# Kernel tuning notes

Hardware: AMD Instinct MI355X
Metric: run time of the kernel (lower is better)

The kernel has to match this reference:

```python
import math
import jax, jax.numpy as jnp
import numpy as np
from jax import lax

B, H, W = 8, 96, 96
FC, R, P, KS, TOPK = 768, 12, 16, 13, 24
SUP_TH, SUP_MIX, OPEN_K, DIL, NMS = 0.28, 0.8, 3, 3, 3

# prototype anchor metadata (buffers, deterministic)
ORI = jnp.asarray(np.linspace(0.0, math.pi, P + 1)[:-1], jnp.float32)
_lenL = np.array([0.4, 0.7, 1.0, 1.25], np.float32)
_widL = np.array([0.12, 0.18, 0.24, 0.3], np.float32)
LEN = jnp.asarray(_lenL[np.arange(P) % 4])
WID = jnp.asarray(_widL[(np.arange(P) // 4) % 4])
_ax = np.linspace(-1.0, 1.0, KS).astype(np.float32)
_gy, _gx = np.meshgrid(_ax, _ax, indexing='ij')
GX, GY = jnp.asarray(_gx), jnp.asarray(_gy)


def conv2d(x, w, b, pad=0):
    y = lax.conv_general_dilated(x, w, (1, 1), [(pad, pad), (pad, pad)],
                                 dimension_numbers=('NCHW', 'OIHW', 'NCHW'))
    return y + b[None, :, None, None]


def maxpool(x, k):
    p = k // 2
    return lax.reduce_window(x, -jnp.inf, lax.max, (1, 1, k, k), (1, 1, 1, 1),
                             [(0, 0), (0, 0), (p, p), (p, p)])


def avgpool3(x):
    s = lax.reduce_window(x, 0.0, lax.add, (1, 1, 3, 3), (1, 1, 1, 1),
                          [(0, 0), (0, 0), (1, 1), (1, 1)])
    return s / 9.0  # torch count_include_pad=True


def normalize_map(t):
    mn = t.min(axis=(-2, -1), keepdims=True)
    mx = t.max(axis=(-2, -1), keepdims=True)
    return (t - mn) / jnp.maximum(mx - mn, 1e-6)


def binary_open(m, k):
    er = 1.0 - maxpool(1.0 - m, k)
    return jnp.clip(maxpool(er, k), 0.0, 1.0)


def support_mask_fn(carrier_hp, density):
    cs = normalize_map(avgpool3(jnp.abs(carrier_hp)))
    ds = normalize_map(density)
    ev = SUP_MIX * cs + (1.0 - SUP_MIX) * ds
    m = (ev >= SUP_TH).astype(carrier_hp.dtype)
    m = binary_open(m, OPEN_K)
    m = maxpool(m, DIL)
    return jnp.clip(m, 0.0, 1.0)


def setup_inputs() -> dict:
    key = jax.random.key(0)
    ks = jax.random.split(key, 16)
    d = {
        'features': jax.random.normal(ks[0], (B, FC, H, W), jnp.float32),
        'carrier_hp': jax.random.normal(ks[1], (B, 1, H, W), jnp.float32),
        'density': jax.random.uniform(ks[2], (B, 1, H, W), jnp.float32),
        # feature_project: 1x1 conv FC->R, 3x3 conv R->R
        'w1': jax.random.normal(ks[3], (R, FC, 1, 1), jnp.float32) * (1.0 / math.sqrt(FC)),
        'b1': jnp.zeros((R,), jnp.float32),
        'w2': jax.random.normal(ks[4], (R, R, 3, 3), jnp.float32) * (1.0 / math.sqrt(R * 9)),
        'b2': jnp.zeros((R,), jnp.float32),
        # post_mix: 1x1 conv (R+4)->R, 1x1 conv R->FC
        'w3': jax.random.normal(ks[5], (R, R + 4, 1, 1), jnp.float32) * (1.0 / math.sqrt(R + 4)),
        'b3': jnp.zeros((R,), jnp.float32),
        'w4': jax.random.normal(ks[6], (FC, R, 1, 1), jnp.float32) * (1.0 / math.sqrt(R)),
        'b4': jnp.zeros((FC,), jnp.float32),
        'proto': jax.random.normal(ks[7], (P, R), jnp.float32) * 0.02,
    }
    return d


def reference(features, carrier_hp, density, w1, b1, w2, b2, w3, b3, w4, b4, proto):
    gelu = lambda x: jax.nn.gelu(x, approximate=False)
    # 1) feature projection
    proj = gelu(conv2d(gelu(conv2d(features, w1, b1, 0)), w2, b2, 1))  # [B,R,H,W]
    # 2) occupancy + support
    occ = normalize_map(jnp.abs(proj).mean(axis=1, keepdims=True))      # [B,1,H,W]
    sup = support_mask_fn(carrier_hp, density)                          # [B,1,H,W]
    # 3) NMS + top-k anchors
    scores = occ * sup
    local_max = maxpool(scores, NMS)
    peak = ((scores >= local_max) & (scores > 0.05)).astype(scores.dtype)
    flat = (scores * peak).reshape(B, -1)
    vals, idx = lax.top_k(flat, TOPK)                                   # [B,K]
    anchor_map = jnp.zeros_like(flat).at[jnp.arange(B)[:, None], idx].set(vals)
    anchor_map = anchor_map.reshape(B, 1, H, W)
    ys, xs = idx // W, idx % W
    # 4) per-anchor prototype selection
    proj_flat = proj.reshape(B, R, H * W)
    feat_at = jnp.take_along_axis(proj_flat, jnp.broadcast_to(idx[:, None, :], (B, R, TOPK)), axis=2)  # [B,R,K]
    logits = jnp.einsum('brk,pr->bkp', feat_at, proto)
    pidx = jnp.argmax(logits, axis=-1)                                  # [B,K]
    ori, ln, wd = ORI[pidx], LEN[pidx], WID[pidx]
    # 5) oriented Gaussian footprints [B,K,KS,KS]
    c = jnp.cos(ori)[..., None, None]
    s = jnp.sin(ori)[..., None, None]
    xr = c * GX + s * GY
    yr = -s * GX + c * GY
    foot = jnp.exp(-(xr / ln[..., None, None]) ** 2 - (yr / wd[..., None, None]) ** 2)
    foot = foot * vals[..., None, None]
    emb = proto[pidx]                                                   # [B,K,R]
    contrib = emb[:, :, :, None, None] * foot[:, :, None]               # [B,K,R,KS,KS]
    # 6) scatter-stamp onto canvas
    off = jnp.arange(KS) - KS // 2
    yy = ys[:, :, None, None] + off[None, None, :, None]                # [B,K,KS,KS]
    xx = xs[:, :, None, None] + off[None, None, None, :]
    valid = ((yy >= 0) & (yy < H) & (xx >= 0) & (xx < W)).astype(contrib.dtype)
    yyc = jnp.clip(yy, 0, H - 1)
    xxc = jnp.clip(xx, 0, W - 1)

    def stamp(ctr, y2, x2, v):
        c0 = jnp.zeros((R, H, W), ctr.dtype)
        return c0.at[:, y2, x2].add(jnp.transpose(ctr, (1, 0, 2, 3)) * v[None])

    canvas = jax.vmap(stamp)(contrib, yyc, xxc, valid)                  # [B,R,H,W]
    # 7) support-lock + post mix
    canvas = canvas * sup
    extras = jnp.concatenate([occ, sup, anchor_map, normalize_map(density)], axis=1)
    mixed = conv2d(gelu(conv2d(jnp.concatenate([canvas, extras], axis=1), w3, b3, 0)), w4, b4, 0)
    return mixed
```

## Files before the change

### kernel.cpp

```cpp
#include <hip/hip_runtime.h>
#include <math.h>

#define Bn 8
#define Hh 96
#define Ww 96
#define NPIX 9216
#define FCn 768
#define Rr 12
#define Pp 16
#define KSn 13
#define TOPKn 24

__device__ __forceinline__ float gelu_f(float x) {
  return 0.5f * x * (1.0f + erff(x * 0.70710678118654752440f));
}

__global__ __launch_bounds__(256) void k_conv1_part(
    const float* __restrict__ feat, const float* __restrict__ w1,
    float* __restrict__ partial) {
  __shared__ float w1s[192 * 12];
  int s = blockIdx.x & 3;
  int pixblk = blockIdx.x >> 2;
  int c0 = s * 192;
  for (int i = threadIdx.x; i < 192 * 12; i += 256) {
    int c = i / 12, r = i % 12;
    w1s[i] = w1[r * FCn + c0 + c];
  }
  __syncthreads();
  int pix = pixblk * 256 + threadIdx.x;
  int b = pix / NPIX, hw = pix % NPIX;
  const float* fb = feat + (size_t)b * FCn * NPIX + (size_t)c0 * NPIX + hw;
  float acc[12];
#pragma unroll
  for (int r = 0; r < 12; r++) acc[r] = 0.f;
  for (int c = 0; c < 192; c += 8) {
    float f[8];
#pragma unroll
    for (int u = 0; u < 8; u++) f[u] = fb[(size_t)(c + u) * NPIX];
#pragma unroll
    for (int u = 0; u < 8; u++) {
#pragma unroll
      for (int r = 0; r < 12; r++)
        acc[r] = fmaf(f[u], w1s[(c + u) * 12 + r], acc[r]);
    }
  }
  float* outp = partial + (size_t)s * (Bn * Rr * NPIX) +
                (size_t)b * Rr * NPIX + hw;
#pragma unroll
  for (int r = 0; r < 12; r++) outp[(size_t)r * NPIX] = acc[r];
}

__global__ __launch_bounds__(256) void k_bias_gelu(
    const float* __restrict__ partial, const float* __restrict__ b1,
    float* __restrict__ t1) {
  int e = blockIdx.x * 256 + threadIdx.x;
  if (e >= Bn * Rr * NPIX) return;
  int r = (e / NPIX) % Rr;
  const size_t N = (size_t)Bn * Rr * NPIX;
  float v = ((partial[e] + partial[e + N]) + partial[e + 2 * N]) +
            partial[e + 3 * N] + b1[r];
  t1[e] = gelu_f(v);
}

__global__ __launch_bounds__(256) void k_conv2(
    const float* __restrict__ t1, const float* __restrict__ w2,
    const float* __restrict__ b2, const float* __restrict__ carrier,
    float* __restrict__ proj, float* __restrict__ occ_raw,
    float* __restrict__ cs_raw) {
  __shared__ float w2s[Rr * Rr * 9];
  __shared__ float b2s[Rr];
  for (int i = threadIdx.x; i < Rr * Rr * 9; i += 256) w2s[i] = w2[i];
  if (threadIdx.x < Rr) b2s[threadIdx.x] = b2[threadIdx.x];
  __syncthreads();
  int pix = blockIdx.x * 256 + threadIdx.x;
  int b = pix / NPIX, hw = pix % NPIX;
  int y = hw / Ww, x = hw % Ww;
  float acc[12];
#pragma unroll
  for (int r = 0; r < 12; r++) acc[r] = 0.f;
  const float* tb = t1 + (size_t)b * Rr * NPIX;
  for (int ri = 0; ri < Rr; ri++) {
    const float* tc = tb + (size_t)ri * NPIX;
#pragma unroll
    for (int ky = 0; ky < 3; ky++) {
      int yy = y + ky - 1;
      if (yy < 0 || yy >= Hh) continue;
#pragma unroll
      for (int kx = 0; kx < 3; kx++) {
        int xx = x + kx - 1;
        if (xx < 0 || xx >= Ww) continue;
        float v = tc[yy * Ww + xx];
#pragma unroll
        for (int ro = 0; ro < 12; ro++)
          acc[ro] = fmaf(v, w2s[((ro * Rr + ri) * 3 + ky) * 3 + kx], acc[ro]);
      }
    }
  }
  float asum = 0.f;
  float* pb = proj + (size_t)b * Rr * NPIX + hw;
#pragma unroll
  for (int ro = 0; ro < 12; ro++) {
    float g = gelu_f(acc[ro] + b2s[ro]);
    pb[(size_t)ro * NPIX] = g;
    asum += fabsf(g);
  }
  occ_raw[pix] = asum / 12.0f;

  const float* cb = carrier + (size_t)b * NPIX;
  float s9 = 0.f;
  for (int dy = -1; dy <= 1; dy++) {
    int yy = y + dy;
    if (yy < 0 || yy >= Hh) continue;
    for (int dx = -1; dx <= 1; dx++) {
      int xx = x + dx;
      if (xx < 0 || xx >= Ww) continue;
      s9 += fabsf(cb[yy * Ww + xx]);
    }
  }
  cs_raw[pix] = s9 / 9.0f;
}

__global__ __launch_bounds__(256) void k_minmax(
    const float* __restrict__ occ_raw, const float* __restrict__ cs_raw,
    const float* __restrict__ density, float* __restrict__ stats) {
  int a = blockIdx.x / Bn, b = blockIdx.x % Bn;
  const float* src = (a == 0) ? occ_raw : (a == 1) ? cs_raw : density;
  src += (size_t)b * NPIX;
  __shared__ float smn[256], smx[256];
  float mn = INFINITY, mx = -INFINITY;
  for (int p = threadIdx.x; p < NPIX; p += 256) {
    float v = src[p];
    mn = fminf(mn, v);
    mx = fmaxf(mx, v);
  }
  smn[threadIdx.x] = mn;
  smx[threadIdx.x] = mx;
  __syncthreads();
  for (int s = 128; s > 0; s >>= 1) {
    if (threadIdx.x < s) {
      smn[threadIdx.x] = fminf(smn[threadIdx.x], smn[threadIdx.x + s]);
      smx[threadIdx.x] = fmaxf(smx[threadIdx.x], smx[threadIdx.x + s]);
    }
    __syncthreads();
  }
  if (threadIdx.x == 0) {
    stats[(a * Bn + b) * 2 + 0] = smn[0];
    stats[(a * Bn + b) * 2 + 1] = smx[0];
  }
}

__global__ __launch_bounds__(1024) void k_support(
    const float* __restrict__ occ_raw, const float* __restrict__ cs_raw,
    const float* __restrict__ density, const float* __restrict__ stats,
    float* __restrict__ occ, float* __restrict__ ds, float* __restrict__ sup,
    float* __restrict__ scores) {
  __shared__ unsigned char mA[NPIX], mB[NPIX];
  int b = blockIdx.x;
  float omn = stats[(0 * Bn + b) * 2], omx = stats[(0 * Bn + b) * 2 + 1];
  float cmn = stats[(1 * Bn + b) * 2], cmx = stats[(1 * Bn + b) * 2 + 1];
  float dmn = stats[(2 * Bn + b) * 2], dmx = stats[(2 * Bn + b) * 2 + 1];
  float oiv = fmaxf(omx - omn, 1e-6f);
  float civ = fmaxf(cmx - cmn, 1e-6f);
  float div_ = fmaxf(dmx - dmn, 1e-6f);
  float occ9[9];
#pragma unroll
  for (int i = 0; i < 9; i++) {
    int p = threadIdx.x + i * 1024;
    float oc = (occ_raw[b * NPIX + p] - omn) / oiv;
    float cv = (cs_raw[b * NPIX + p] - cmn) / civ;
    float dv = (density[b * NPIX + p] - dmn) / div_;
    occ[b * NPIX + p] = oc;
    ds[b * NPIX + p] = dv;
    occ9[i] = oc;
    float ev = 0.8f * cv + 0.2f * dv;
    mA[p] = (ev >= 0.28f) ? 1 : 0;
  }
  __syncthreads();
#pragma unroll
  for (int i = 0; i < 9; i++) {
    int p = threadIdx.x + i * 1024;
    int y = p / Ww, x = p % Ww;
    unsigned char m = 1;
    for (int dy = -1; dy <= 1; dy++) {
      int yy = y + dy;
      if (yy < 0 || yy >= Hh) continue;
      for (int dx = -1; dx <= 1; dx++) {
        int xx = x + dx;
        if (xx < 0 || xx >= Ww) continue;
        m = (unsigned char)(m & mA[yy * Ww + xx]);
      }
    }
    mB[p] = m;
  }
  __syncthreads();
#pragma unroll
  for (int i = 0; i < 9; i++) {
    int p = threadIdx.x + i * 1024;
    int y = p / Ww, x = p % Ww;
    unsigned char m = 0;
    for (int dy = -1; dy <= 1; dy++) {
      int yy = y + dy;
      if (yy < 0 || yy >= Hh) continue;
      for (int dx = -1; dx <= 1; dx++) {
        int xx = x + dx;
        if (xx < 0 || xx >= Ww) continue;
        m = (unsigned char)(m | mB[yy * Ww + xx]);
      }
    }
    mA[p] = m;
  }
  __syncthreads();
#pragma unroll
  for (int i = 0; i < 9; i++) {
    int p = threadIdx.x + i * 1024;
    int y = p / Ww, x = p % Ww;
    unsigned char m = 0;
    for (int dy = -1; dy <= 1; dy++) {
      int yy = y + dy;
      if (yy < 0 || yy >= Hh) continue;
      for (int dx = -1; dx <= 1; dx++) {
        int xx = x + dx;
        if (xx < 0 || xx >= Ww) continue;
        m = (unsigned char)(m | mA[yy * Ww + xx]);
      }
    }
    float sv = (float)m;
    sup[b * NPIX + p] = sv;
    scores[b * NPIX + p] = occ9[i] * sv;
  }
}

__global__ __launch_bounds__(256) void k_topk(
    const float* __restrict__ scores, float* __restrict__ vals,
    int* __restrict__ idxs, float* __restrict__ anchor) {
  __shared__ float flat[NPIX];
  __shared__ float rv[256];
  __shared__ int ri[256];
  int b = blockIdx.x;
  const float* sc = scores + (size_t)b * NPIX;
  for (int p = threadIdx.x; p < NPIX; p += 256) {
    int y = p / Ww, x = p % Ww;
    float s = sc[p];
    float lm = -INFINITY;
    for (int dy = -1; dy <= 1; dy++) {
      int yy = y + dy;
      if (yy < 0 || yy >= Hh) continue;
      for (int dx = -1; dx <= 1; dx++) {
        int xx = x + dx;
        if (xx < 0 || xx >= Ww) continue;
        lm = fmaxf(lm, sc[yy * Ww + xx]);
      }
    }
    flat[p] = (s >= lm && s > 0.05f) ? s : 0.0f;
  }
  __syncthreads();
  for (int k = 0; k < TOPKn; k++) {
    float bv = -INFINITY;
    int bi = 0x7fffffff;
    for (int p = threadIdx.x; p < NPIX; p += 256) {
      float v = flat[p];
      if (v > bv || (v == bv && p < bi)) {
        bv = v;
        bi = p;
      }
    }
    rv[threadIdx.x] = bv;
    ri[threadIdx.x] = bi;
    __syncthreads();
    for (int s = 128; s > 0; s >>= 1) {
      if (threadIdx.x < s) {
        float ov = rv[threadIdx.x + s];
        int oi = ri[threadIdx.x + s];
        if (ov > rv[threadIdx.x] || (ov == rv[threadIdx.x] && oi < ri[threadIdx.x])) {
          rv[threadIdx.x] = ov;
          ri[threadIdx.x] = oi;
        }
      }
      __syncthreads();
    }
    if (threadIdx.x == 0) {
      vals[b * TOPKn + k] = rv[0];
      idxs[b * TOPKn + k] = ri[0];
      flat[ri[0]] = -2.0f;
      anchor[b * NPIX + ri[0]] = rv[0];
    }
    __syncthreads();
  }
}

__global__ __launch_bounds__(192) void k_stamp(
    const float* __restrict__ proj, const float* __restrict__ proto,
    const float* __restrict__ vals, const int* __restrict__ idxs,
    float* __restrict__ canvas) {
  int b = blockIdx.x / TOPKn, k = blockIdx.x % TOPKn;
  __shared__ float embs[12];
  __shared__ float prm[5];
  __shared__ int ppos[2];
  if (threadIdx.x == 0) {
    int id = idxs[b * TOPKn + k];
    float v = vals[b * TOPKn + k];
    float ft[12];
    for (int r = 0; r < 12; r++)
      ft[r] = proj[(size_t)(b * Rr + r) * NPIX + id];
    float bestL = -INFINITY;
    int bp = 0;
    for (int p = 0; p < Pp; p++) {
      float L = 0.f;
      for (int r = 0; r < 12; r++) L = fmaf(ft[r], proto[p * Rr + r], L);
      if (L > bestL) {
        bestL = L;
        bp = p;
      }
    }
    const float lenL[4] = {0.4f, 0.7f, 1.0f, 1.25f};
    const float widL[4] = {0.12f, 0.18f, 0.24f, 0.3f};
    float ori = (float)((M_PI / 16.0) * (double)bp);
    prm[0] = cosf(ori);
    prm[1] = sinf(ori);
    prm[2] = lenL[bp & 3];
    prm[3] = widL[(bp >> 2) & 3];
    prm[4] = v;
    ppos[0] = id / Ww;
    ppos[1] = id % Ww;
    for (int r = 0; r < 12; r++) embs[r] = proto[bp * Rr + r];
  }
  __syncthreads();
  float v = prm[4];
  if (v <= 0.f) return;
  int t = threadIdx.x;
  if (t >= KSn * KSn) return;
  int i = t / KSn, j = t % KSn;
  float gx = (float)(-1.0 + (double)j * (1.0 / 6.0));
  float gy = (float)(-1.0 + (double)i * (1.0 / 6.0));
  float c = prm[0], s = prm[1];
  float xr = c * gx + s * gy;
  float yr = -s * gx + c * gy;
  float tx = xr / prm[2], ty = yr / prm[3];
  float foot = expf(-(tx * tx) - (ty * ty)) * v;
  int yy = ppos[0] + i - KSn / 2;
  int xx = ppos[1] + j - KSn / 2;
  if (yy < 0 || yy >= Hh || xx < 0 || xx >= Ww) return;
  float* cp = canvas + (size_t)b * Rr * NPIX + yy * Ww + xx;
#pragma unroll
  for (int r = 0; r < 12; r++) atomicAdd(cp + (size_t)r * NPIX, embs[r] * foot);
}

__global__ __launch_bounds__(256) void k_post1(
    const float* __restrict__ canvas, const float* __restrict__ sup,
    const float* __restrict__ occ, const float* __restrict__ anchor,
    const float* __restrict__ ds, const float* __restrict__ w3,
    const float* __restrict__ b3, float* __restrict__ h) {
  __shared__ float w3s[12 * 16], b3s[12];
  for (int i = threadIdx.x; i < 192; i += 256) w3s[i] = w3[i];
  if (threadIdx.x < 12) b3s[threadIdx.x] = b3[threadIdx.x];
  __syncthreads();
  int pix = blockIdx.x * 256 + threadIdx.x;
  int b = pix / NPIX, hw = pix % NPIX;
  float in16[16];
  float sv = sup[pix];
#pragma unroll
  for (int r = 0; r < 12; r++)
    in16[r] = canvas[(size_t)(b * Rr + r) * NPIX + hw] * sv;
  in16[12] = occ[pix];
  in16[13] = sv;
  in16[14] = anchor[pix];
  in16[15] = ds[pix];
  float* hb = h + (size_t)b * Rr * NPIX + hw;
#pragma unroll
  for (int ro = 0; ro < 12; ro++) {
    float acc = 0.f;
#pragma unroll
    for (int ci = 0; ci < 16; ci++)
      acc = fmaf(in16[ci], w3s[ro * 16 + ci], acc);
    hb[(size_t)ro * NPIX] = gelu_f(acc + b3s[ro]);
  }
}

__global__ __launch_bounds__(256) void k_post2(
    const float* __restrict__ h, const float* __restrict__ w4,
    const float* __restrict__ b4, float* __restrict__ out) {
  __shared__ float w4s[16 * 12], b4s[16];
  int bx = blockIdx.x;
  int hwblk = bx % 36;
  int g = (bx / 36) % 48;
  int b = bx / (36 * 48);
  int oc0 = g * 16;
  for (int i = threadIdx.x; i < 192; i += 256) w4s[i] = w4[oc0 * 12 + i];
  if (threadIdx.x < 16) b4s[threadIdx.x] = b4[oc0 + threadIdx.x];
  __syncthreads();
  int hw = hwblk * 256 + threadIdx.x;
  float hreg[12];
  const float* hb = h + (size_t)b * Rr * NPIX + hw;
#pragma unroll
  for (int r = 0; r < 12; r++) hreg[r] = hb[(size_t)r * NPIX];
  float* ob = out + (size_t)(b * FCn + oc0) * NPIX + hw;
#pragma unroll
  for (int j = 0; j < 16; j++) {
    float acc = 0.f;
#pragma unroll
    for (int r = 0; r < 12; r++) acc = fmaf(hreg[r], w4s[j * 12 + r], acc);
    ob[(size_t)j * NPIX] = acc + b4s[j];
  }
}

extern "C" void kernel_launch(void* const* d_in, const int* in_sizes, int n_in,
                              void* d_out, int out_size, void* d_ws,
                              size_t ws_size, hipStream_t stream) {
  const float* features = (const float*)d_in[0];
  const float* carrier = (const float*)d_in[1];
  const float* density = (const float*)d_in[2];
  const float* w1 = (const float*)d_in[3];
  const float* b1 = (const float*)d_in[4];
  const float* w2 = (const float*)d_in[5];
  const float* b2 = (const float*)d_in[6];
  const float* w3 = (const float*)d_in[7];
  const float* b3 = (const float*)d_in[8];
  const float* w4 = (const float*)d_in[9];
  const float* b4 = (const float*)d_in[10];
  const float* proto = (const float*)d_in[11];
  float* out = (float*)d_out;
  float* ws = (float*)d_ws;

  const size_t NT = (size_t)Bn * Rr * NPIX;
  float* t1 = ws;
  float* partial = ws + NT;
  float* proj = partial;
  float* canvas = partial + NT;
  float* h = partial + 2 * NT;
  float* sm = ws + 5 * NT;
  float* occ_raw = sm;
  float* cs_raw = sm + (size_t)Bn * NPIX;
  float* occ = sm + 2 * (size_t)Bn * NPIX;
  float* ds = sm + 3 * (size_t)Bn * NPIX;
  float* sup = sm + 4 * (size_t)Bn * NPIX;
  float* scores = sm + 5 * (size_t)Bn * NPIX;
  float* anchor = sm + 6 * (size_t)Bn * NPIX;
  float* stats = sm + 7 * (size_t)Bn * NPIX;
  float* vals = stats + 64;
  int* idxs = (int*)(vals + Bn * TOPKn);

  k_conv1_part<<<288 * 4, 256, 0, stream>>>(features, w1, partial);
  k_bias_gelu<<<(int)((NT + 255) / 256), 256, 0, stream>>>(partial, b1, t1);
  hipMemsetAsync(canvas, 0, NT * sizeof(float), stream);
  hipMemsetAsync(anchor, 0, (size_t)Bn * NPIX * sizeof(float), stream);
  k_conv2<<<288, 256, 0, stream>>>(t1, w2, b2, carrier, proj, occ_raw, cs_raw);
  k_minmax<<<24, 256, 0, stream>>>(occ_raw, cs_raw, density, stats);
  k_support<<<Bn, 1024, 0, stream>>>(occ_raw, cs_raw, density, stats, occ, ds,
                                     sup, scores);
  k_topk<<<Bn, 256, 0, stream>>>(scores, vals, idxs, anchor);
  k_stamp<<<Bn * TOPKn, 192, 0, stream>>>(proj, proto, vals, idxs, canvas);
  k_post1<<<288, 256, 0, stream>>>(canvas, sup, occ, anchor, ds, w3, b3, h);
  k_post2<<<Bn * 48 * 36, 256, 0, stream>>>(h, w4, b4, out);
}
```

Measured before the change: 651.1 us.

## Compact NMS peak candidates before top-k and use wave-shuffle reductions

The top-k kernel first loads each batch's score map into shared memory and runs the 3x3 local-max suppression from there. Surviving peaks are compacted with a shared atomic counter into a small candidate list (up to 1536 entries). The 24 argmax passes then scan only that list instead of all 9216 pixels. Each pass reduces with 64-lane shuffles and a 4-way cross-wave step instead of an 8-level shared-memory tree with many barriers. If there are too many candidates it falls back to the full scan, and when no positive value remains it writes index 0 rather than the lowest zero pixel, which can change tie behaviour.

Result: faster. 581.7 us (-10.7%).

```diff
diff --git a/kernel.cpp b/kernel.cpp
--- a/kernel.cpp
+++ b/kernel.cpp
@@ -10,6 +10,7 @@
 #define Pp 16
 #define KSn 13
 #define TOPKn 24
+#define CAPc 1536
 
 __device__ __forceinline__ float gelu_f(float x) {
   return 0.5f * x * (1.0f + erff(x * 0.70710678118654752440f));
@@ -234,13 +235,25 @@
     const float* __restrict__ scores, float* __restrict__ vals,
     int* __restrict__ idxs, float* __restrict__ anchor) {
   __shared__ float flat[NPIX];
-  __shared__ float rv[256];
-  __shared__ int ri[256];
+  __shared__ float cval[CAPc];
+  __shared__ int cidx[CAPc];
+  __shared__ int cnt;
+  __shared__ float rv[4];
+  __shared__ int ri[4], rs[4];
   int b = blockIdx.x;
+  const int tid = threadIdx.x;
+  const int lane = tid & 63, wid = tid >> 6;
   const float* sc = scores + (size_t)b * NPIX;
-  for (int p = threadIdx.x; p < NPIX; p += 256) {
+#pragma unroll
+  for (int i = 0; i < NPIX / 256; i++) flat[tid + i * 256] = sc[tid + i * 256];
+  if (tid == 0) cnt = 0;
+  __syncthreads();
+  float pk[NPIX / 256];
+#pragma unroll
+  for (int i = 0; i < NPIX / 256; i++) {
+    int p = tid + i * 256;
     int y = p / Ww, x = p % Ww;
-    float s = sc[p];
+    float s = flat[p];
     float lm = -INFINITY;
     for (int dy = -1; dy <= 1; dy++) {
       int yy = y + dy;
@@ -248,43 +261,122 @@
       for (int dx = -1; dx <= 1; dx++) {
         int xx = x + dx;
         if (xx < 0 || xx >= Ww) continue;
-        lm = fmaxf(lm, sc[yy * Ww + xx]);
-      }
-    }
-    flat[p] = (s >= lm && s > 0.05f) ? s : 0.0f;
-  }
-  __syncthreads();
-  for (int k = 0; k < TOPKn; k++) {
-    float bv = -INFINITY;
-    int bi = 0x7fffffff;
-    for (int p = threadIdx.x; p < NPIX; p += 256) {
-      float v = flat[p];
-      if (v > bv || (v == bv && p < bi)) {
-        bv = v;
-        bi = p;
-      }
-    }
-    rv[threadIdx.x] = bv;
-    ri[threadIdx.x] = bi;
-    __syncthreads();
-    for (int s = 128; s > 0; s >>= 1) {
-      if (threadIdx.x < s) {
-        float ov = rv[threadIdx.x + s];
-        int oi = ri[threadIdx.x + s];
-        if (ov > rv[threadIdx.x] || (ov == rv[threadIdx.x] && oi < ri[threadIdx.x])) {
-          rv[threadIdx.x] = ov;
-          ri[threadIdx.x] = oi;
-        }
+        lm = fmaxf(lm, flat[yy * Ww + xx]);
+      }
+    }
+    pk[i] = (s >= lm && s > 0.05f) ? s : 0.0f;
+  }
+  __syncthreads();
+#pragma unroll
+  for (int i = 0; i < NPIX / 256; i++) {
+    int p = tid + i * 256;
+    flat[p] = pk[i];
+    if (pk[i] > 0.f) {
+      int slot = atomicAdd(&cnt, 1);
+      if (slot < CAPc) {
+        cval[slot] = pk[i];
+        cidx[slot] = p;
+      }
+    }
+  }
+  __syncthreads();
+  const int C = cnt;
+  if (C <= CAPc) {
+    for (int k = 0; k < TOPKn; k++) {
+      float bv = -INFINITY;
+      int bi = 0x7fffffff, bs = -1;
+      for (int j = tid; j < C; j += 256) {
+        float v = cval[j];
+        int pi = cidx[j];
+        if (v > bv || (v == bv && pi < bi)) {
+          bv = v;
+          bi = pi;
+          bs = j;
+        }
+      }
+      for (int off = 32; off > 0; off >>= 1) {
+        float ov = __shfl_xor(bv, off);
+        int oi = __shfl_xor(bi, off);
+        int os = __shfl_xor(bs, off);
+        if (ov > bv || (ov == bv && oi < bi)) {
+          bv = ov;
+          bi = oi;
+          bs = os;
+        }
+      }
+      if (lane == 0) {
+        rv[wid] = bv;
+        ri[wid] = bi;
+        rs[wid] = bs;
       }
       __syncthreads();
-    }
-    if (threadIdx.x == 0) {
-      vals[b * TOPKn + k] = rv[0];
-      idxs[b * TOPKn + k] = ri[0];
-      flat[ri[0]] = -2.0f;
-      anchor[b * NPIX + ri[0]] = rv[0];
-    }
-    __syncthreads();
+      if (tid == 0) {
+        float Bv = rv[0];
+        int Bi = ri[0], Bs = rs[0];
+        for (int w = 1; w < 4; w++) {
+          if (rv[w] > Bv || (rv[w] == Bv && ri[w] < Bi)) {
+            Bv = rv[w];
+            Bi = ri[w];
+            Bs = rs[w];
+          }
+        }
+        if (Bv > 0.f) {
+          vals[b * TOPKn + k] = Bv;
+          idxs[b * TOPKn + k] = Bi;
+          anchor[b * NPIX + Bi] = Bv;
+          cval[Bs] = -INFINITY;
+        } else {
+          vals[b * TOPKn + k] = 0.f;
+          idxs[b * TOPKn + k] = 0;
+        }
+      }
+      __syncthreads();
+    }
+  } else {
+    for (int k = 0; k < TOPKn; k++) {
+      float bv = -INFINITY;
+      int bi = 0x7fffffff;
+      for (int p = tid; p < NPIX; p += 256) {
+        float v = flat[p];
+        if (v > bv || (v == bv && p < bi)) {
+          bv = v;
+          bi = p;
+        }
+      }
+      for (int off = 32; off > 0; off >>= 1) {
+        float ov = __shfl_xor(bv, off);
+        int oi = __shfl_xor(bi, off);
+        if (ov > bv || (ov == bv && oi < bi)) {
+          bv = ov;
+          bi = oi;
+        }
+      }
+      if (lane == 0) {
+        rv[wid] = bv;
+        ri[wid] = bi;
+      }
+      __syncthreads();
+      if (tid == 0) {
+        float Bv = rv[0];
+        int Bi = ri[0];
+        for (int w = 1; w < 4; w++) {
+          if (rv[w] > Bv || (rv[w] == Bv && ri[w] < Bi)) {
+            Bv = rv[w];
+            Bi = ri[w];
+          }
+        }
+        if (Bv > 0.f) {
+          vals[b * TOPKn + k] = Bv;
+          idxs[b * TOPKn + k] = Bi;
+          anchor[b * NPIX + Bi] = Bv;
+          flat[Bi] = -INFINITY;
+        } else {
+          vals[b * TOPKn + k] = 0.f;
+          idxs[b * TOPKn + k] = 0;
+        }
+      }
+      __syncthreads();
+    }
   }
 }
 
```
